# Performance work log

Measured on AMD Instinct MI355X. Metric: run time of the kernel, lower is better.

## Reference

```python
import jax, jax.numpy as jnp
import numpy as np

EMB = 128
HEAD = 8
QKV = 16
SQRT_EMB = 11.313708498984761
CLIP = 10.0
B, P, N = 64, 100, 1000


def setup_inputs() -> dict:
    key = jax.random.key(0)
    ks = jax.random.split(key, 12)
    encoded_last_node = jax.random.normal(ks[0], (B, P, EMB), jnp.float32)
    load = jax.random.uniform(ks[1], (B, P), jnp.float32)
    time = jax.random.uniform(ks[2], (B, P), jnp.float32)
    cur_dist = jax.random.uniform(ks[3], (B, P, N), jnp.float32)
    mask_bits = jax.random.uniform(ks[4], (B, P, N)) < 0.1
    ninf_mask = jnp.where(mask_bits, -1e9, 0.0).astype(jnp.float32)
    noise = jax.random.uniform(ks[5], (B, P, N), jnp.float32)
    encoded_nodes = jax.random.normal(ks[6], (B, N, EMB), jnp.float32)
    s = 1.0 / np.sqrt(EMB)
    Wq = jax.random.uniform(ks[7], (EMB + 2, HEAD * QKV), jnp.float32, -s, s)
    Wk = jax.random.uniform(ks[8], (EMB, HEAD * QKV), jnp.float32, -s, s)
    Wv = jax.random.uniform(ks[9], (EMB, HEAD * QKV), jnp.float32, -s, s)
    Wc = jax.random.uniform(ks[10], (HEAD * QKV, EMB), jnp.float32, -s, s)
    bc = jax.random.uniform(ks[11], (EMB,), jnp.float32, -s, s)
    return {"encoded_last_node": encoded_last_node, "load": load, "time": time,
            "cur_dist": cur_dist, "ninf_mask": ninf_mask, "noise": noise,
            "encoded_nodes": encoded_nodes, "Wq": Wq, "Wk": Wk, "Wv": Wv,
            "Wc": Wc, "bc": bc}


def _heads(x):
    # (B, n, H*D) -> (B, H, n, D)
    b, n, _ = x.shape
    return x.reshape(b, n, HEAD, QKV).transpose(0, 2, 1, 3)


def reference(encoded_last_node, load, time, cur_dist, ninf_mask, noise,
              encoded_nodes, Wq, Wk, Wv, Wc, bc):
    # set_kv
    k = _heads(encoded_nodes @ Wk)   # (B,H,N,D)
    v = _heads(encoded_nodes @ Wv)   # (B,H,N,D)

    # query from last node + load + time
    input_cat = jnp.concatenate(
        [encoded_last_node, load[:, :, None], time[:, :, None]], axis=2)
    q = _heads(input_cat @ Wq)       # (B,H,P,D)

    # multi-head attention with rank3 ninf mask
    score = jnp.einsum('bhpd,bhnd->bhpn', q, k) / jnp.sqrt(
        jnp.asarray(QKV, jnp.float32))
    score = score + ninf_mask[:, None, :, :]
    weights = jax.nn.softmax(score, axis=3)
    out = jnp.einsum('bhpn,bhnd->bhpd', weights, v)
    out_concat = out.transpose(0, 2, 1, 3).reshape(B, P, HEAD * QKV)
    mh_atten_out = out_concat @ Wc + bc            # (B,P,EMB)

    # single-head pointer logits
    score2 = jnp.einsum('bpe,bne->bpn', mh_atten_out, encoded_nodes)
    score_scaled = score2 / SQRT_EMB

    # heuristic / noise blend
    st_cost = cur_dist + cur_dist
    raw_heuristic = -jnp.log(st_cost + 1e-6)
    a = 1.0 / (1.0 + 2.0 ** ((100.0 - N) / 50.0))
    b = 1.0 - a
    mixed_signal = a * raw_heuristic + b * noise
    s = score_scaled + mixed_signal
    score_clipped = CLIP * jnp.tanh(s)
    score_masked = score_clipped + ninf_mask
    probs = jax.nn.softmax(score_masked, axis=2)
    return probs
```

## Files before the change

kernel.cpp:

```cpp
#include <hip/hip_runtime.h>
#include <hip/hip_bf16.h>

#define B_   64
#define P_   100
#define N_   1000
#define EMB_ 128
#define HEAD_ 8
#define QKV_ 16
#define QT   4

constexpr double kTwoPowNeg18 = 3.814697265625e-06;
constexpr double kA_d = 1.0 / (1.0 + kTwoPowNeg18);

#define KEEP4(v) asm volatile("" : "+v"((v).x), "+v"((v).y), "+v"((v).z), "+v"((v).w))

__global__ __launch_bounds__(256) void kv_proj(
    const float* __restrict__ en, const float* __restrict__ Wk,
    const float* __restrict__ Wv, float* __restrict__ K2, float* __restrict__ V2)
{
    __shared__ __align__(16) float e_s[64][128];
    const int t  = threadIdx.x;
    const int j  = t & 63;
    const int rb = (t >> 6) * 16;
    const int r0 = blockIdx.x * 64;

    {
        const float4* src = (const float4*)(en + (size_t)r0 * 128);
        float4* dst = (float4*)&e_s[0][0];
        #pragma unroll
        for (int k = 0; k < 8; ++k) dst[t + 256 * k] = src[t + 256 * k];
    }
    __syncthreads();

    float ak0[16], ak1[16], av0[16], av1[16];
    #pragma unroll
    for (int r = 0; r < 16; ++r) { ak0[r] = 0.f; ak1[r] = 0.f; av0[r] = 0.f; av1[r] = 0.f; }

    for (int i4 = 0; i4 < 32; ++i4) {
        float wk0[4], wk1[4], wv0[4], wv1[4];
        #pragma unroll
        for (int c = 0; c < 4; ++c) {
            const int rowi = (4 * i4 + c) * 128;
            wk0[c] = Wk[rowi + j];
            wk1[c] = Wk[rowi + j + 64];
            wv0[c] = Wv[rowi + j];
            wv1[c] = Wv[rowi + j + 64];
        }
        #pragma unroll
        for (int r = 0; r < 16; ++r) {
            const float4 e4 = *(const float4*)&e_s[rb + r][4 * i4];
            ak0[r] = fmaf(e4.x, wk0[0], fmaf(e4.y, wk0[1],
                     fmaf(e4.z, wk0[2], fmaf(e4.w, wk0[3], ak0[r]))));
            ak1[r] = fmaf(e4.x, wk1[0], fmaf(e4.y, wk1[1],
                     fmaf(e4.z, wk1[2], fmaf(e4.w, wk1[3], ak1[r]))));
            av0[r] = fmaf(e4.x, wv0[0], fmaf(e4.y, wv0[1],
                     fmaf(e4.z, wv0[2], fmaf(e4.w, wv0[3], av0[r]))));
            av1[r] = fmaf(e4.x, wv1[0], fmaf(e4.y, wv1[1],
                     fmaf(e4.z, wv1[2], fmaf(e4.w, wv1[3], av1[r]))));
        }
    }

    const int h0 = j >> 4, d0 = j & 15;
    const int h1 = (j + 64) >> 4, d1 = j & 15;
    #pragma unroll
    for (int r = 0; r < 16; ++r) {
        const int row = r0 + rb + r;
        const int bb = row / N_;
        const int n = row - bb * N_;
        const size_t base = ((size_t)bb * HEAD_ * N_ + n) * 16;
        K2[base + (size_t)h0 * N_ * 16 + d0] = ak0[r];
        K2[base + (size_t)h1 * N_ * 16 + d1] = ak1[r];
        V2[base + (size_t)h0 * N_ * 16 + d0] = av0[r];
        V2[base + (size_t)h1 * N_ * 16 + d1] = av1[r];
    }
}

__global__ __launch_bounds__(128) void q_proj(
    const float* __restrict__ eln, const float* __restrict__ load_,
    const float* __restrict__ time_, const float* __restrict__ Wq,
    float* __restrict__ Q)
{
    __shared__ __align__(16) float e_s[8][132];
    const int j  = threadIdx.x;
    const int r0 = blockIdx.x * 8;

    #pragma unroll
    for (int r = 0; r < 8; ++r) {
        const int row = r0 + r;
        e_s[r][j] = eln[(size_t)row * 128 + j];
        if (j == 0) {
            e_s[r][128] = load_[row];
            e_s[r][129] = time_[row];
        }
    }
    __syncthreads();

    float a[8];
    #pragma unroll
    for (int r = 0; r < 8; ++r) a[r] = 0.f;

    for (int i4 = 0; i4 < 32; ++i4) {
        float w4[4];
        #pragma unroll
        for (int c = 0; c < 4; ++c) w4[c] = Wq[(4 * i4 + c) * 128 + j];
        #pragma unroll
        for (int r = 0; r < 8; ++r) {
            const float4 e4 = *(const float4*)&e_s[r][4 * i4];
            a[r] = fmaf(e4.x, w4[0], fmaf(e4.y, w4[1],
                   fmaf(e4.z, w4[2], fmaf(e4.w, w4[3], a[r]))));
        }
    }
    #pragma unroll
    for (int i = 128; i < 130; ++i) {
        const float w = Wq[i * 128 + j];
        #pragma unroll
        for (int r = 0; r < 8; ++r)
            a[r] = fmaf(e_s[r][i], w, a[r]);
    }

    #pragma unroll
    for (int r = 0; r < 8; ++r)
        Q[(size_t)(r0 + r) * 128 + j] = a[r];
}

__global__ __launch_bounds__(256) void attn_heads(
    const float* __restrict__ K2, const float* __restrict__ V2,
    const float* __restrict__ Q, const float* __restrict__ ninf,
    float* __restrict__ out_g)
{
    __shared__ __align__(16) float sc[QT][1008];
    __shared__ __align__(16) float q_s[QT][16];
    __shared__ __align__(16) float part_s[4][QT][16];
    __shared__ float invden_s[QT];

    const int blk = blockIdx.x;
    const int h   = blk & 7;
    const int j9  = blk >> 3;
    const int pt  = j9 % 25;
    const int b   = j9 / 25;
    const int bp0 = b * P_ + pt * QT;
    const int t    = threadIdx.x;
    const int lane = t & 63;
    const int wv   = t >> 6;

    if (t < 64) q_s[t >> 4][t & 15] =
        Q[(size_t)(bp0 + (t >> 4)) * 128 + h * 16 + (t & 15)];
    __syncthreads();

    float qr[QT][16];
    #pragma unroll
    for (int q = 0; q < QT; ++q)
        #pragma unroll
        for (int c = 0; c < 4; ++c)
            *(float4*)&qr[q][4 * c] = *(const float4*)&q_s[q][4 * c];

    const float* nf0 = ninf + (size_t)bp0 * N_;
    float msk[QT][4];
    #pragma unroll
    for (int i = 0; i < 4; ++i) {
        const int n = t + 256 * i;
        if (n < N_) {
            #pragma unroll
            for (int q = 0; q < QT; ++q) msk[q][i] = nf0[q * N_ + n];
        }
    }

    const float* Kh = K2 + (size_t)(b * HEAD_ + h) * N_ * 16;
    #pragma unroll
    for (int i = 0; i < 4; ++i) {
        const int n = t + 256 * i;
        if (n < N_) {
            const float4* kr = (const float4*)(Kh + (size_t)n * 16);
            const float4 k0 = kr[0], k1 = kr[1], k2 = kr[2], k3 = kr[3];
            #pragma unroll
            for (int q = 0; q < QT; ++q) {
                float d = k0.x * qr[q][0]  + k0.y * qr[q][1]
                        + k0.z * qr[q][2]  + k0.w * qr[q][3]
                        + k1.x * qr[q][4]  + k1.y * qr[q][5]
                        + k1.z * qr[q][6]  + k1.w * qr[q][7]
                        + k2.x * qr[q][8]  + k2.y * qr[q][9]
                        + k2.z * qr[q][10] + k2.w * qr[q][11]
                        + k3.x * qr[q][12] + k3.y * qr[q][13]
                        + k3.z * qr[q][14] + k3.w * qr[q][15];
                sc[q][n] = d * 0.25f + msk[q][i];
            }
        }
    }
    __syncthreads();

    {
        const int q = wv;
        float m = -INFINITY;
        for (int n = lane; n < N_; n += 64) m = fmaxf(m, sc[q][n]);
        #pragma unroll
        for (int off = 32; off > 0; off >>= 1) m = fmaxf(m, __shfl_xor(m, off));
        float s = 0.f;
        for (int n = lane; n < N_; n += 64) {
            const float e = __expf(sc[q][n] - m);
            sc[q][n] = e;
            s += e;
        }
        #pragma unroll
        for (int off = 32; off > 0; off >>= 1) s += __shfl_xor(s, off);
        if (lane == 0) invden_s[q] = 1.f / s;
    }
    __syncthreads();

    {
        const int c = lane & 3, g = lane >> 2;
        const float* Vh = V2 + (size_t)(b * HEAD_ + h) * N_ * 16 + 4 * c;
        const int n0 = wv * 250;
        float4 a0 = {0.f, 0.f, 0.f, 0.f}, a1 = a0, a2 = a0, a3 = a0;
        #pragma unroll 4
        for (int i = 0; i < 16; ++i) {
            const int nn = 16 * i + g;
            if (nn < 250) {
                const int n = n0 + nn;
                const float4 v4 = *(const float4*)(Vh + (size_t)n * 16);
                const float w0 = sc[0][n], w1 = sc[1][n];
                const float w2 = sc[2][n], w3 = sc[3][n];
                a0.x = fmaf(w0, v4.x, a0.x); a0.y = fmaf(w0, v4.y, a0.y);
                a0.z = fmaf(w0, v4.z, a0.z); a0.w = fmaf(w0, v4.w, a0.w);
                a1.x = fmaf(w1, v4.x, a1.x); a1.y = fmaf(w1, v4.y, a1.y);
                a1.z = fmaf(w1, v4.z, a1.z); a1.w = fmaf(w1, v4.w, a1.w);
                a2.x = fmaf(w2, v4.x, a2.x); a2.y = fmaf(w2, v4.y, a2.y);
                a2.z = fmaf(w2, v4.z, a2.z); a2.w = fmaf(w2, v4.w, a2.w);
                a3.x = fmaf(w3, v4.x, a3.x); a3.y = fmaf(w3, v4.y, a3.y);
                a3.z = fmaf(w3, v4.z, a3.z); a3.w = fmaf(w3, v4.w, a3.w);
            }
        }
        #pragma unroll
        for (int off = 4; off <= 32; off <<= 1) {
            a0.x += __shfl_xor(a0.x, off); a0.y += __shfl_xor(a0.y, off);
            a0.z += __shfl_xor(a0.z, off); a0.w += __shfl_xor(a0.w, off);
            a1.x += __shfl_xor(a1.x, off); a1.y += __shfl_xor(a1.y, off);
            a1.z += __shfl_xor(a1.z, off); a1.w += __shfl_xor(a1.w, off);
            a2.x += __shfl_xor(a2.x, off); a2.y += __shfl_xor(a2.y, off);
            a2.z += __shfl_xor(a2.z, off); a2.w += __shfl_xor(a2.w, off);
            a3.x += __shfl_xor(a3.x, off); a3.y += __shfl_xor(a3.y, off);
            a3.z += __shfl_xor(a3.z, off); a3.w += __shfl_xor(a3.w, off);
        }
        if (g == 0) {
            *(float4*)&part_s[wv][0][4 * c] = a0;
            *(float4*)&part_s[wv][1][4 * c] = a1;
            *(float4*)&part_s[wv][2][4 * c] = a2;
            *(float4*)&part_s[wv][3][4 * c] = a3;
        }
    }
    __syncthreads();

    if (t < 64) {
        const int q = t >> 4, d = t & 15;
        const float s = part_s[0][q][d] + part_s[1][q][d]
                      + part_s[2][q][d] + part_s[3][q][d];
        out_g[(size_t)(bp0 + q) * 128 + h * 16 + d] = s * invden_s[q];
    }
}

__global__ __launch_bounds__(256) void ptr_epilogue(
    const float* __restrict__ out_g, const float* __restrict__ en,
    const float* __restrict__ Wc, const float* __restrict__ bc,
    const float* __restrict__ cur_dist, const float* __restrict__ ninf,
    const float* __restrict__ noise, float* __restrict__ probs)
{
    __shared__ __align__(16) float sc[QT][1008];
    __shared__ __align__(16) float out_s[QT][128];
    __shared__ __align__(16) float mh_s[QT][128];

    const int blk  = blockIdx.x;
    const int rX   = blk & 7;
    const int j9   = blk >> 3;
    const int pt   = j9 % 25;
    const int b    = (j9 / 25) * 8 + rX;
    const int bp0  = b * P_ + pt * QT;
    const int t    = threadIdx.x;
    const int lane = t & 63;
    const int wv   = t >> 6;

    if (t < 128)
        ((float4*)&out_s[0][0])[t] = ((const float4*)(out_g + (size_t)bp0 * 128))[t];
    __syncthreads();

    {
        const int e = t & 127, qh = t >> 7;
        float a0 = bc[e], a1 = a0;
        for (int i = 0; i < 128; ++i) {
            const float w = Wc[i * 128 + e];
            a0 = fmaf(out_s[qh][i], w, a0);
            a1 = fmaf(out_s[qh + 2][i], w, a1);
        }
        mh_s[qh][e] = a0;
        mh_s[qh + 2][e] = a1;
    }
    __syncthreads();

    {
        const int k16 = lane & 15, g = lane >> 4;
        float4 mh0[QT], mh1[QT];
        #pragma unroll
        for (int q = 0; q < QT; ++q) {
            mh0[q] = *(const float4*)&mh_s[q][k16 * 8];
            mh1[q] = *(const float4*)&mh_s[q][k16 * 8 + 4];
            KEEP4(mh0[q]);
            KEEP4(mh1[q]);
        }
        const float* enb = en + (size_t)b * N_ * 128;
        #pragma unroll 2
        for (int nb = 4 * wv; nb < N_; nb += 16) {
            const int n = nb + g;
            const float4* er = (const float4*)(enb + (size_t)n * 128 + k16 * 8);
            const float4 e0 = er[0], e1 = er[1];
            float acc[QT];
            #pragma unroll
            for (int q = 0; q < QT; ++q) {
                acc[q] = e0.x * mh0[q].x + e0.y * mh0[q].y
                       + e0.z * mh0[q].z + e0.w * mh0[q].w
                       + e1.x * mh1[q].x + e1.y * mh1[q].y
                       + e1.z * mh1[q].z + e1.w * mh1[q].w;
            }
            #pragma unroll
            for (int q = 0; q < QT; ++q) {
                float v = acc[q];
                v += __shfl_xor(v, 1);
                v += __shfl_xor(v, 2);
                v += __shfl_xor(v, 4);
                v += __shfl_xor(v, 8);
                if (k16 == 0) sc[q][n] = v;
            }
        }
    }
    __syncthreads();

    {
        const int q  = wv;
        const int bp = bp0 + q;
        const float* cd = cur_dist + (size_t)bp * N_;
        const float* nz = noise    + (size_t)bp * N_;
        const float* nf = ninf     + (size_t)bp * N_;
        const float A   = (float)kA_d;
        const float Bc2 = (float)(1.0 - kA_d);

        float m = -INFINITY;
        for (int n = lane; n < N_; n += 64) {
            const float s2 = sc[q][n] / 11.3137085f;
            const float st = cd[n] + cd[n];
            const float rh = -logf(st + 1e-6f);
            const float s  = s2 + A * rh + Bc2 * nz[n];
            const float sm = 10.f * tanhf(s) + nf[n];
            sc[q][n] = sm;
            m = fmaxf(m, sm);
        }
        #pragma unroll
        for (int off = 32; off > 0; off >>= 1) m = fmaxf(m, __shfl_xor(m, off));

        float s = 0.f;
        for (int n = lane; n < N_; n += 64) {
            const float e = __expf(sc[q][n] - m);
            sc[q][n] = e;
            s += e;
        }
        #pragma unroll
        for (int off = 32; off > 0; off >>= 1) s += __shfl_xor(s, off);

        const float inv = 1.f / s;
        float* out = probs + (size_t)bp * N_;
        for (int n = lane; n < N_; n += 64) out[n] = sc[q][n] * inv;
    }
}

extern "C" void kernel_launch(void* const* d_in, const int* in_sizes, int n_in,
                              void* d_out, int out_size, void* d_ws, size_t ws_size,
                              hipStream_t stream)
{
    const float* eln      = (const float*)d_in[0];
    const float* load_    = (const float*)d_in[1];
    const float* time_    = (const float*)d_in[2];
    const float* cur_dist = (const float*)d_in[3];
    const float* ninf     = (const float*)d_in[4];
    const float* noise    = (const float*)d_in[5];
    const float* en       = (const float*)d_in[6];
    const float* Wq       = (const float*)d_in[7];
    const float* Wk       = (const float*)d_in[8];
    const float* Wv       = (const float*)d_in[9];
    const float* Wc       = (const float*)d_in[10];
    const float* bc       = (const float*)d_in[11];
    float* probs = (float*)d_out;

    float* K2    = (float*)d_ws;
    float* V2    = K2 + (size_t)B_ * HEAD_ * N_ * 16;
    float* Q     = V2 + (size_t)B_ * HEAD_ * N_ * 16;
    float* out_g = Q  + (size_t)B_ * P_ * 128;

    kv_proj<<<(B_ * N_) / 64, 256, 0, stream>>>(en, Wk, Wv, K2, V2);
    q_proj<<<(B_ * P_) / 8, 128, 0, stream>>>(eln, load_, time_, Wq, Q);
    attn_heads<<<B_ * HEAD_ * (P_ / QT), 256, 0, stream>>>(K2, V2, Q, ninf, out_g);
    ptr_epilogue<<<(B_ * P_) / QT, 256, 0, stream>>>(out_g, en, Wc, bc,
                                                     cur_dist, ninf, noise, probs);
}
```

Measured before the change: 488.2 us.

## Compute pointer logits one node per thread and use fast tanh/log intrinsics

Restructures the pointer-score dot product so each thread owns up to four nodes and accumulates full 128-wide dot products against the four query rows read from shared memory. This removes the per-node cross-lane shuffle reductions of the old 16-lane split. Each thread now reads node rows with a large stride, so global loads are no longer coalesced across lanes, which could cost bandwidth or cache efficiency. The epilogue also replaces logf, tanhf and the division with __logf, a clamped exp-based tanh and a reciprocal multiply, trading a little accuracy for cheaper arithmetic.

Result: slower. 522.8 us (+7.1%).

```diff
diff --git a/kernel.cpp b/kernel.cpp
--- a/kernel.cpp
+++ b/kernel.cpp
@@ -11,8 +11,6 @@
 
 constexpr double kTwoPowNeg18 = 3.814697265625e-06;
 constexpr double kA_d = 1.0 / (1.0 + kTwoPowNeg18);
-
-#define KEEP4(v) asm volatile("" : "+v"((v).x), "+v"((v).y), "+v"((v).z), "+v"((v).w))
 
 __global__ __launch_bounds__(256) void kv_proj(
     const float* __restrict__ en, const float* __restrict__ Wk,
@@ -295,38 +293,50 @@
     __syncthreads();
 
     {
-        const int k16 = lane & 15, g = lane >> 4;
-        float4 mh0[QT], mh1[QT];
+        const float* enb = en + (size_t)b * N_ * 128;
+        const bool has4 = (t + 768 < N_);
+        const float4* e0p = (const float4*)(enb + (size_t)t * 128);
+        const float4* e1p = (const float4*)(enb + (size_t)(t + 256) * 128);
+        const float4* e2p = (const float4*)(enb + (size_t)(t + 512) * 128);
+        const float4* e3p = (const float4*)(enb + (size_t)(has4 ? t + 768 : t) * 128);
+        const float4* m0 = (const float4*)mh_s[0];
+        const float4* m1 = (const float4*)mh_s[1];
+        const float4* m2 = (const float4*)mh_s[2];
+        const float4* m3 = (const float4*)mh_s[3];
+
+        float acc[4][QT];
+        #pragma unroll
+        for (int r = 0; r < 4; ++r)
+            #pragma unroll
+            for (int q = 0; q < QT; ++q) acc[r][q] = 0.f;
+
+        #pragma unroll 2
+        for (int i = 0; i < 32; ++i) {
+            const float4 w0 = m0[i], w1 = m1[i], w2 = m2[i], w3 = m3[i];
+            const float4 r0 = e0p[i], r1 = e1p[i], r2 = e2p[i], r3 = e3p[i];
+            acc[0][0] += r0.x*w0.x + r0.y*w0.y + r0.z*w0.z + r0.w*w0.w;
+            acc[0][1] += r0.x*w1.x + r0.y*w1.y + r0.z*w1.z + r0.w*w1.w;
+            acc[0][2] += r0.x*w2.x + r0.y*w2.y + r0.z*w2.z + r0.w*w2.w;
+            acc[0][3] += r0.x*w3.x + r0.y*w3.y + r0.z*w3.z + r0.w*w3.w;
+            acc[1][0] += r1.x*w0.x + r1.y*w0.y + r1.z*w0.z + r1.w*w0.w;
+            acc[1][1] += r1.x*w1.x + r1.y*w1.y + r1.z*w1.z + r1.w*w1.w;
+            acc[1][2] += r1.x*w2.x + r1.y*w2.y + r1.z*w2.z + r1.w*w2.w;
+            acc[1][3] += r1.x*w3.x + r1.y*w3.y + r1.z*w3.z + r1.w*w3.w;
+            acc[2][0] += r2.x*w0.x + r2.y*w0.y + r2.z*w0.z + r2.w*w0.w;
+            acc[2][1] += r2.x*w1.x + r2.y*w1.y + r2.z*w1.z + r2.w*w1.w;
+            acc[2][2] += r2.x*w2.x + r2.y*w2.y + r2.z*w2.z + r2.w*w2.w;
+            acc[2][3] += r2.x*w3.x + r2.y*w3.y + r2.z*w3.z + r2.w*w3.w;
+            acc[3][0] += r3.x*w0.x + r3.y*w0.y + r3.z*w0.z + r3.w*w0.w;
+            acc[3][1] += r3.x*w1.x + r3.y*w1.y + r3.z*w1.z + r3.w*w1.w;
+            acc[3][2] += r3.x*w2.x + r3.y*w2.y + r3.z*w2.z + r3.w*w2.w;
+            acc[3][3] += r3.x*w3.x + r3.y*w3.y + r3.z*w3.z + r3.w*w3.w;
+        }
         #pragma unroll
         for (int q = 0; q < QT; ++q) {
-            mh0[q] = *(const float4*)&mh_s[q][k16 * 8];
-            mh1[q] = *(const float4*)&mh_s[q][k16 * 8 + 4];
-            KEEP4(mh0[q]);
-            KEEP4(mh1[q]);
-        }
-        const float* enb = en + (size_t)b * N_ * 128;
-        #pragma unroll 2
-        for (int nb = 4 * wv; nb < N_; nb += 16) {
-            const int n = nb + g;
-            const float4* er = (const float4*)(enb + (size_t)n * 128 + k16 * 8);
-            const float4 e0 = er[0], e1 = er[1];
-            float acc[QT];
-            #pragma unroll
-            for (int q = 0; q < QT; ++q) {
-                acc[q] = e0.x * mh0[q].x + e0.y * mh0[q].y
-                       + e0.z * mh0[q].z + e0.w * mh0[q].w
-                       + e1.x * mh1[q].x + e1.y * mh1[q].y
-                       + e1.z * mh1[q].z + e1.w * mh1[q].w;
-            }
-            #pragma unroll
-            for (int q = 0; q < QT; ++q) {
-                float v = acc[q];
-                v += __shfl_xor(v, 1);
-                v += __shfl_xor(v, 2);
-                v += __shfl_xor(v, 4);
-                v += __shfl_xor(v, 8);
-                if (k16 == 0) sc[q][n] = v;
-            }
+            sc[q][t]       = acc[0][q];
+            sc[q][t + 256] = acc[1][q];
+            sc[q][t + 512] = acc[2][q];
+            if (has4) sc[q][t + 768] = acc[3][q];
         }
     }
     __syncthreads();
@@ -339,14 +349,18 @@
         const float* nf = ninf     + (size_t)bp * N_;
         const float A   = (float)kA_d;
         const float Bc2 = (float)(1.0 - kA_d);
+        const float invSqrtEmb = 0.0883883476483184406f;
 
         float m = -INFINITY;
         for (int n = lane; n < N_; n += 64) {
-            const float s2 = sc[q][n] / 11.3137085f;
+            const float s2 = sc[q][n] * invSqrtEmb;
             const float st = cd[n] + cd[n];
-            const float rh = -logf(st + 1e-6f);
-            const float s  = s2 + A * rh + Bc2 * nz[n];
-            const float sm = 10.f * tanhf(s) + nf[n];
+            const float rh = -__logf(st + 1e-6f);
+            float s = s2 + A * rh + Bc2 * nz[n];
+            s = fminf(fmaxf(s, -12.f), 12.f);
+            const float e2 = __expf(s + s);
+            const float cl = 10.f * __fdividef(e2 - 1.f, e2 + 1.f);
+            const float sm = cl + nf[n];
             sc[q][n] = sm;
             m = fmaxf(m, sm);
         }
```
